# Kernel optimization log

Measured on AMD Instinct MI355X. Metric: run time of the kernel, lower is better.

The kernel has to match this reference:

```python
import jax, jax.numpy as jnp
import numpy as np

N, NFEAT, NHID, NCLASS, NLAYERS = 8192, 512, 128, 40, 3
NEG = -9e15

def _sparse_adj(key, n, density=0.002):
    u = jax.random.uniform(key, (n, n), dtype=jnp.float32)
    return jnp.where(u < density, u / density, 0.0)

def setup_inputs() -> dict:
    key = jax.random.key(0)
    ks = jax.random.split(key, 12)
    return {
        "x": jax.random.normal(ks[0], (N, NFEAT), dtype=jnp.float32),
        "adj1": _sparse_adj(ks[1], N),
        "adj2": _sparse_adj(ks[2], N),
        "adj_att": _sparse_adj(ks[3], N),
        "fc1_w": jax.random.normal(ks[4], (NLAYERS, NHID, NFEAT), dtype=jnp.float32) * (1.0 / np.sqrt(NFEAT)),
        "fc1_b": jnp.zeros((NLAYERS, NHID), jnp.float32),
        "Q_w": jax.random.normal(ks[5], (NLAYERS - 1, NHID, NHID), dtype=jnp.float32) * (1.0 / np.sqrt(NHID)),
        "Q_b": jnp.zeros((NLAYERS - 1, NHID), jnp.float32),
        "K_w": jax.random.normal(ks[6], (NLAYERS - 1, NHID, NHID), dtype=jnp.float32) * (1.0 / np.sqrt(NHID)),
        "K_b": jnp.zeros((NLAYERS - 1, NHID), jnp.float32),
        "hop_select": jnp.ones((NLAYERS,), jnp.float32),
        "w": jnp.ones((NLAYERS - 1, 2), jnp.float32),
        "clf_w": jax.random.normal(ks[7], (NCLASS, NHID * NLAYERS), dtype=jnp.float32) * (1.0 / np.sqrt(NHID * NLAYERS)),
        "clf_b": jnp.zeros((NCLASS,), jnp.float32),
    }

def _l2_normalize(x, eps=1e-12):
    # F.normalize(x, p=2, dim=1)
    n = jnp.sqrt(jnp.sum(x * x, axis=1, keepdims=True))
    return x / jnp.maximum(n, eps)

def reference(x, adj1, adj2, adj_att, fc1_w, fc1_b, Q_w, Q_b, K_w, K_b,
              hop_select, w, clf_w, clf_b):
    adj_list = [None, adj1, adj2]
    mask = jax.nn.softmax(hop_select)  # hop selection weights, shape [nlayers]
    outs = []
    for i in range(NLAYERS):
        tmp = x @ fc1_w[i].T + fc1_b[i]  # [N, nhid]
        if adj_list[i] is not None:
            adj = adj_list[i]
            W_att = jax.nn.softmax(w[i - 1])  # [2]
            tmp_att = adj_att @ tmp           # [N, nhid]
            # GCN1: linear then propagate with adj_att (act='None')
            Q = adj_att @ (tmp_att @ Q_w[i - 1].T + Q_b[i - 1])
            K = adj_att @ (tmp_att @ K_w[i - 1].T + K_b[i - 1])
            scores = Q @ K.T                  # [N, N]
            scores = jnp.where(adj > 0, scores, NEG)
            attention = jax.nn.softmax(scores, axis=-1) * W_att[0] + adj * W_att[1]
            tmp = attention @ tmp             # [N, nhid]
        tmp = _l2_normalize(tmp)
        outs.append(mask[i] * tmp)
    final = jnp.concatenate(outs, axis=1)     # [N, nhid*nlayers]
    out = jax.nn.relu(final) @ clf_w.T + clf_b  # dropout is identity in eval
    return jax.nn.log_softmax(out, axis=1)
```

## Files before the change

kernel.cpp:

```cpp
#include <hip/hip_runtime.h>
#include <hip/hip_bf16.h>

#define NN     8192
#define NF4    2048
#define NFEAT  512
#define NHID   128
#define NCLASS 40
#define NLAY   3
#define CAPA   128
#define FSZ    ((size_t)NN * NHID)

typedef float f32x4 __attribute__((ext_vector_type(4)));

__global__ __launch_bounds__(256, 4) void k_scan_fc1(
    const float* __restrict__ x, const float* __restrict__ fc1w, const float* __restrict__ fc1b,
    const float* __restrict__ adjA, const float* __restrict__ adj1, const float* __restrict__ adj2,
    const float* __restrict__ hop, const float* __restrict__ w,
    float* __restrict__ tmps, float* __restrict__ f_mask, float* __restrict__ f_watt,
    float* __restrict__ colsum, float* __restrict__ rowsumA,
    int* __restrict__ cnts, int* __restrict__ colsArr, float* __restrict__ valsArr)
{
    __shared__ float smem[6400];
    __shared__ int s_lcnt;
    __shared__ float s_lsum;
    const int bx = blockIdx.x, plane = blockIdx.y, tid = threadIdx.x;

    if (bx < 128) {
        float* As = smem;
        float* Bs = smem + 2176;
        const int tx = tid & 15, ty = tid >> 4;
        const int bm = bx * 64;
        const int layer = plane;
        const int bn = layer * 128;
        float acc[4][8] = {};

        for (int kt = 0; kt < NFEAT; kt += 32) {
            #pragma unroll
            for (int it = 0; it < 2; ++it) {
                int L = tid + it * 256;
                int r = L >> 3, c4 = (L & 7) * 4;
                f32x4 va = *reinterpret_cast<const f32x4*>(&x[(size_t)(bm + r) * NFEAT + kt + c4]);
                As[(c4 + 0) * 68 + r] = va[0];
                As[(c4 + 1) * 68 + r] = va[1];
                As[(c4 + 2) * 68 + r] = va[2];
                As[(c4 + 3) * 68 + r] = va[3];
            }
            #pragma unroll
            for (int it = 0; it < 4; ++it) {
                int L = tid + it * 256;
                int r = L >> 3, c4 = (L & 7) * 4;
                f32x4 vb = *reinterpret_cast<const f32x4*>(&fc1w[(size_t)(bn + r) * NFEAT + kt + c4]);
                Bs[(c4 + 0) * 132 + r] = vb[0];
                Bs[(c4 + 1) * 132 + r] = vb[1];
                Bs[(c4 + 2) * 132 + r] = vb[2];
                Bs[(c4 + 3) * 132 + r] = vb[3];
            }
            __syncthreads();
            #pragma unroll
            for (int kk = 0; kk < 32; ++kk) {
                f32x4 ra  = *reinterpret_cast<const f32x4*>(&As[kk * 68 + ty * 4]);
                f32x4 rb0 = *reinterpret_cast<const f32x4*>(&Bs[kk * 132 + tx * 4]);
                f32x4 rb1 = *reinterpret_cast<const f32x4*>(&Bs[kk * 132 + tx * 4 + 64]);
                #pragma unroll
                for (int i = 0; i < 4; ++i) {
                    #pragma unroll
                    for (int j = 0; j < 4; ++j) {
                        acc[i][j]     = fmaf(ra[i], rb0[j], acc[i][j]);
                        acc[i][j + 4] = fmaf(ra[i], rb1[j], acc[i][j + 4]);
                    }
                }
            }
            __syncthreads();
        }
        const float* bofs = fc1b + bn;
        #pragma unroll
        for (int i = 0; i < 4; ++i) {
            int m = bm + ty * 4 + i;
            #pragma unroll
            for (int j = 0; j < 8; ++j) {
                int lc = (j < 4) ? (tx * 4 + j) : (64 + tx * 4 + (j - 4));
                tmps[(size_t)layer * FSZ + (size_t)m * NHID + lc] = acc[i][j] + bofs[lc];
            }
        }
    } else if (bx < 128 + NN) {
        const int row = bx - 128, mat = plane;
        const float* adj = (mat == 0) ? adjA : (mat == 1 ? adj1 : adj2);
        if (tid == 0) { s_lcnt = 0; s_lsum = 0.f; }
        __syncthreads();
        const f32x4* arow = reinterpret_cast<const f32x4*>(adj + (size_t)row * NN);
        int* rc = colsArr + (size_t)(mat * NN + row) * CAPA;
        float* rv = valsArr + (size_t)(mat * NN + row) * CAPA;

        f32x4 v[8];
        #pragma unroll
        for (int i = 0; i < 8; ++i)
            v[i] = __builtin_nontemporal_load(&arow[tid + (i << 8)]);

        float ls = 0.f;
        #pragma unroll
        for (int i = 0; i < 8; ++i) {
            const int c4 = tid + (i << 8);
            #pragma unroll
            for (int k = 0; k < 4; ++k) {
                if (v[i][k] > 0.f) {
                    int p = atomicAdd(&s_lcnt, 1);
                    if (p < CAPA) { rc[p] = c4 * 4 + k; rv[p] = v[i][k]; }
                    ls += v[i][k];
                }
            }
        }
        if (mat == 0 && ls != 0.f) atomicAdd(&s_lsum, ls);
        __syncthreads();
        if (tid == 0) {
            cnts[mat * NN + row] = s_lcnt < CAPA ? s_lcnt : CAPA;
            if (mat == 0) rowsumA[row] = s_lsum;
        }
    } else if (plane == 0) {
        colsum[tid] = 0.f;
        if (tid == 0) {
            float m = fmaxf(fmaxf(hop[0], hop[1]), hop[2]);
            float e0 = expf(hop[0] - m), e1 = expf(hop[1] - m), e2 = expf(hop[2] - m);
            float s = e0 + e1 + e2;
            f_mask[0] = e0 / s; f_mask[1] = e1 / s; f_mask[2] = e2 / s;
            for (int l = 0; l < 2; ++l) {
                float a = w[2 * l], b = w[2 * l + 1];
                float mm = fmaxf(a, b);
                float ea = expf(a - mm), eb = expf(b - mm);
                float ss = ea + eb;
                f_watt[2 * l] = ea / ss; f_watt[2 * l + 1] = eb / ss;
            }
        }
    }
}

__global__ __launch_bounds__(128) void k_spmm_cs(
    const int* __restrict__ cnts, const int* __restrict__ colsArr, const float* __restrict__ valsArr,
    const float* __restrict__ tmps, float* __restrict__ tmp_att, float* __restrict__ colsum)
{
    int bx = blockIdx.x, L = blockIdx.y, t = threadIdx.x;
    if (bx >= NN) {
        int c = bx - NN;
        const float* X = tmps + (size_t)(L + 1) * FSZ + (size_t)c * 128 * NHID;
        float a = 0.f;
        for (int r = 0; r < 128; ++r) a += X[(size_t)r * NHID + t];
        atomicAdd(&colsum[L * NHID + t], a);
        return;
    }
    int row = bx;
    const float* X = tmps + (size_t)(L + 1) * FSZ;
    float* Y = tmp_att + (size_t)L * FSZ;
    __shared__ int sc[CAPA];
    __shared__ float sv[CAPA];
    int n = cnts[row];
    for (int p = t; p < n; p += 128) { sc[p] = colsArr[(size_t)row * CAPA + p]; sv[p] = valsArr[(size_t)row * CAPA + p]; }
    __syncthreads();
    float a0 = 0.f, a1 = 0.f, a2 = 0.f, a3 = 0.f;
    int p = 0;
    for (; p + 4 <= n; p += 4) {
        a0 = fmaf(sv[p],     X[(size_t)sc[p]     * NHID + t], a0);
        a1 = fmaf(sv[p + 1], X[(size_t)sc[p + 1] * NHID + t], a1);
        a2 = fmaf(sv[p + 2], X[(size_t)sc[p + 2] * NHID + t], a2);
        a3 = fmaf(sv[p + 3], X[(size_t)sc[p + 3] * NHID + t], a3);
    }
    for (; p < n; ++p) a0 = fmaf(sv[p], X[(size_t)sc[p] * NHID + t], a0);
    Y[(size_t)row * NHID + t] = (a0 + a1) + (a2 + a3);
}

__global__ __launch_bounds__(256, 2) void k_t2qkm(
    const int* __restrict__ cnts, const int* __restrict__ colsArr, const float* __restrict__ valsArr,
    const float* __restrict__ tmp_att, const float* __restrict__ Qw, const float* __restrict__ Kw,
    const float* __restrict__ Qb, const float* __restrict__ Kb,
    const float* __restrict__ rowsumA, float* __restrict__ QKm)
{
    __shared__ float AsT[128 * 64];
    __shared__ float Bs[128 * 64];
    const int tid = threadIdx.x;
    const int bm = blockIdx.x * 64, Lz = blockIdx.y;
    const float* X = tmp_att + (size_t)Lz * FSZ;

    {
        const int lrow = tid >> 2, coff = (tid & 3) * 32;
        const int row = bm + lrow;
        f32x4 acc[8] = {};
        const int n = cnts[row];
        const int* rc = colsArr + (size_t)row * CAPA;
        const float* rv = valsArr + (size_t)row * CAPA;
        for (int p = 0; p < n; ++p) {
            int c = rc[p];
            float v = rv[p];
            const f32x4* src = reinterpret_cast<const f32x4*>(X + (size_t)c * NHID + coff);
            #pragma unroll
            for (int j = 0; j < 8; ++j) {
                f32x4 s = src[j];
                acc[j][0] = fmaf(v, s[0], acc[j][0]);
                acc[j][1] = fmaf(v, s[1], acc[j][1]);
                acc[j][2] = fmaf(v, s[2], acc[j][2]);
                acc[j][3] = fmaf(v, s[3], acc[j][3]);
            }
        }
        #pragma unroll
        for (int j = 0; j < 8; ++j)
            #pragma unroll
            for (int q = 0; q < 4; ++q)
                AsT[(coff + j * 4 + q) * 64 + lrow] = acc[j][q];
    }
    __syncthreads();

    const int tx = tid & 15, ty = tid >> 4;
    float rs[4];
    #pragma unroll
    for (int i = 0; i < 4; ++i) rs[i] = rowsumA[bm + ty * 4 + i];
    float* C = QKm + (size_t)Lz * NN * 256;

    for (int ch = 0; ch < 4; ++ch) {
        const int bn = ch * 64;
        const float* Bp; const float* bp; int bc;
        if (bn < 128) { Bp = Qw + (size_t)Lz * NHID * NHID; bp = Qb + (size_t)Lz * NHID; bc = bn; }
        else          { Bp = Kw + (size_t)Lz * NHID * NHID; bp = Kb + (size_t)Lz * NHID; bc = bn - 128; }
        {
            int r = tid >> 2, c0 = (tid & 3) * 32;
            #pragma unroll
            for (int j = 0; j < 8; ++j) {
                f32x4 v = *reinterpret_cast<const f32x4*>(&Bp[(size_t)(bc + r) * NHID + c0 + j * 4]);
                #pragma unroll
                for (int q = 0; q < 4; ++q) Bs[(c0 + j * 4 + q) * 64 + r] = v[q];
            }
        }
        __syncthreads();
        float acc[4][4] = {};
        #pragma unroll 8
        for (int kk = 0; kk < 128; ++kk) {
            f32x4 ra = *reinterpret_cast<const f32x4*>(&AsT[kk * 64 + ty * 4]);
            f32x4 rb = *reinterpret_cast<const f32x4*>(&Bs[kk * 64 + tx * 4]);
            #pragma unroll
            for (int i = 0; i < 4; ++i)
                #pragma unroll
                for (int j = 0; j < 4; ++j)
                    acc[i][j] = fmaf(ra[i], rb[j], acc[i][j]);
        }
        #pragma unroll
        for (int i = 0; i < 4; ++i) {
            int m = bm + ty * 4 + i;
            #pragma unroll
            for (int j = 0; j < 4; ++j) {
                int nc = bn + tx * 4 + j;
                C[(size_t)m * 256 + nc] = acc[i][j] + rs[i] * bp[bc + tx * 4 + j];
            }
        }
        __syncthreads();
    }
}

__global__ __launch_bounds__(256) void k_attn(
    const int* __restrict__ cnts, const int* __restrict__ colsArr, const float* __restrict__ valsArr,
    const float* __restrict__ QKm, const float* __restrict__ tmps,
    const float* __restrict__ colsum, const float* __restrict__ watt,
    const float* __restrict__ mask, float* __restrict__ outsb)
{
    int row = blockIdx.x, L = blockIdx.y, t = threadIdx.x;
    const float* QK = QKm + (size_t)L * NN * 256;
    const float* T = tmps + (size_t)(L + 1) * FSZ;
    const int* rc = colsArr + (size_t)((1 + L) * NN + row) * CAPA;
    const float* rv = valsArr + (size_t)((1 + L) * NN + row) * CAPA;
    __shared__ int cols[CAPA];
    __shared__ float avals[CAPA];
    __shared__ float svals[CAPA];
    __shared__ __align__(16) float qrow[NHID];
    __shared__ float psum[2][NHID];
    __shared__ float ws[4];

    int n = cnts[(1 + L) * NN + row];
    for (int p = t; p < n; p += 256) { cols[p] = rc[p]; avals[p] = rv[p]; }
    if (t < 32) *reinterpret_cast<f32x4*>(&qrow[t * 4]) =
        *reinterpret_cast<const f32x4*>(QK + (size_t)row * 256 + t * 4);
    __syncthreads();

    float W0 = watt[L * 2], W1 = watt[L * 2 + 1];
    float acc = 0.f;

    if (n > 0) {
        int g = t >> 5, sl = t & 31;
        f32x4 qv = *reinterpret_cast<const f32x4*>(&qrow[sl * 4]);
        for (int p = g; p < n; p += 8) {
            f32x4 kv = *reinterpret_cast<const f32x4*>(QK + (size_t)cols[p] * 256 + 128 + sl * 4);
            float s = qv[0] * kv[0] + qv[1] * kv[1] + qv[2] * kv[2] + qv[3] * kv[3];
            #pragma unroll
            for (int m = 16; m; m >>= 1) s += __shfl_xor(s, m);
            if (sl == 0) svals[p] = s;
        }
        __syncthreads();
        if (t < 64) {
            float mx = -3.0e38f;
            for (int p = t; p < n; p += 64) mx = fmaxf(mx, svals[p]);
            #pragma unroll
            for (int m = 32; m; m >>= 1) mx = fmaxf(mx, __shfl_xor(mx, m));
            float ss = 0.f;
            for (int p = t; p < n; p += 64) ss += expf(svals[p] - mx);
            #pragma unroll
            for (int m = 32; m; m >>= 1) ss += __shfl_xor(ss, m);
            float inv = 1.0f / ss;
            for (int p = t; p < n; p += 64) avals[p] = expf(svals[p] - mx) * inv * W0 + avals[p] * W1;
        }
        __syncthreads();
        int half = t >> 7, tt = t & 127;
        float pacc = 0.f;
        for (int p = half; p < n; p += 2) pacc = fmaf(avals[p], T[(size_t)cols[p] * NHID + tt], pacc);
        psum[half][tt] = pacc;
        __syncthreads();
        if (t < 128) acc = psum[0][t] + psum[1][t];
    } else {
        if (t < 128) acc = W0 * (1.0f / (float)NN) * colsum[L * NHID + t];
    }

    float s2 = acc * acc;
    #pragma unroll
    for (int m = 32; m; m >>= 1) s2 += __shfl_xor(s2, m);
    if ((t & 63) == 0) ws[t >> 6] = s2;
    __syncthreads();
    if (t < 128) {
        float d = fmaxf(sqrtf(ws[0] + ws[1]), 1e-12f);
        outsb[(size_t)row * (NHID * NLAY) + (size_t)(L + 1) * NHID + t] = mask[L + 1] * acc / d;
    }
}

__global__ __launch_bounds__(128) void k_clf(
    const float* __restrict__ tmps0, const float* __restrict__ outs,
    const float* __restrict__ Wc, const float* __restrict__ bc,
    const float* __restrict__ mask, float* __restrict__ out)
{
    __shared__ float fin[2][NHID * NLAY];
    const int t = threadIdx.x, wv = t >> 6, lane = t & 63;
    const int row = blockIdx.x * 2 + wv;

    float v0 = tmps0[(size_t)row * NHID + lane];
    float v1 = tmps0[(size_t)row * NHID + 64 + lane];
    float s = v0 * v0 + v1 * v1;
    #pragma unroll
    for (int m = 32; m; m >>= 1) s += __shfl_xor(s, m);
    float d = fmaxf(sqrtf(s), 1e-12f);
    float m0 = mask[0];
    fin[wv][lane]      = fmaxf(m0 * v0 / d, 0.f);
    fin[wv][64 + lane] = fmaxf(m0 * v1 / d, 0.f);
    #pragma unroll
    for (int k = 0; k < 4; ++k)
        fin[wv][128 + k * 64 + lane] = fmaxf(outs[(size_t)row * (NHID * NLAY) + 128 + k * 64 + lane], 0.f);
    __syncthreads();

    float logit = -3.0e38f;
    if (lane < NCLASS) {
        const float* wrow = Wc + (size_t)lane * (NHID * NLAY);
        float a0 = 0.f, a1 = 0.f, a2 = 0.f, a3 = 0.f;
        #pragma unroll 4
        for (int k = 0; k < NHID * NLAY; k += 4) {
            a0 = fmaf(fin[wv][k],     wrow[k],     a0);
            a1 = fmaf(fin[wv][k + 1], wrow[k + 1], a1);
            a2 = fmaf(fin[wv][k + 2], wrow[k + 2], a2);
            a3 = fmaf(fin[wv][k + 3], wrow[k + 3], a3);
        }
        logit = bc[lane] + (a0 + a1) + (a2 + a3);
    }
    float mx = logit;
    #pragma unroll
    for (int m = 32; m; m >>= 1) mx = fmaxf(mx, __shfl_xor(mx, m));
    float e = (lane < NCLASS) ? expf(logit - mx) : 0.f;
    float ssum = e;
    #pragma unroll
    for (int m = 32; m; m >>= 1) ssum += __shfl_xor(ssum, m);
    if (lane < NCLASS) out[(size_t)row * NCLASS + lane] = logit - mx - logf(ssum);
}

extern "C" void kernel_launch(void* const* d_in, const int* in_sizes, int n_in,
                              void* d_out, int out_size, void* d_ws, size_t ws_size,
                              hipStream_t stream) {
    const float* x       = (const float*)d_in[0];
    const float* adj1    = (const float*)d_in[1];
    const float* adj2    = (const float*)d_in[2];
    const float* adj_att = (const float*)d_in[3];
    const float* fc1_w   = (const float*)d_in[4];
    const float* fc1_b   = (const float*)d_in[5];
    const float* Q_w     = (const float*)d_in[6];
    const float* Q_b     = (const float*)d_in[7];
    const float* K_w     = (const float*)d_in[8];
    const float* K_b     = (const float*)d_in[9];
    const float* hop     = (const float*)d_in[10];
    const float* w       = (const float*)d_in[11];
    const float* clf_w   = (const float*)d_in[12];
    const float* clf_b   = (const float*)d_in[13];

    float* W = (float*)d_ws;
    float* f_mask   = W;
    float* f_watt   = W + 4;
    float* f_colsum = W + 8;
    float* rowsumA  = W + 264;
    float* tmps     = W + 264 + NN;
    float* outsb    = tmps + 3 * FSZ;
    float* tmp_att  = outsb + 3 * FSZ;
    float* QKm      = tmp_att + 2 * FSZ;
    float* csr_vals = QKm + 4 * FSZ;
    int*   csr_cols = (int*)(csr_vals + 3 * FSZ);
    int*   csr_cnt  = csr_cols + 3 * FSZ;

    size_t need = (size_t)((char*)(csr_cnt + 3 * NN) - (char*)d_ws);
    if (ws_size < need) return;

    k_scan_fc1<<<dim3(NN + 129, 3), 256, 0, stream>>>(
        x, fc1_w, fc1_b, adj_att, adj1, adj2, hop, w,
        tmps, f_mask, f_watt, f_colsum, rowsumA, csr_cnt, csr_cols, csr_vals);

    k_spmm_cs<<<dim3(NN + 64, 2), 128, 0, stream>>>(
        csr_cnt, csr_cols, csr_vals, tmps, tmp_att, f_colsum);

    k_t2qkm<<<dim3(NN / 64, 2), 256, 0, stream>>>(
        csr_cnt, csr_cols, csr_vals, tmp_att, Q_w, K_w, Q_b, K_b, rowsumA, QKm);

    k_attn<<<dim3(NN, 2), 256, 0, stream>>>(
        csr_cnt, csr_cols, csr_vals, QKm, tmps, f_colsum, f_watt, f_mask, outsb);

    k_clf<<<NN / 2, 128, 0, stream>>>(tmps, outsb, clf_w, clf_b, f_mask, (float*)d_out);
}
```

Before: 356.4 us.

## Move adj1/adj2 scans into the QK stage and fuse attention with classifier

The first kernel now scans only adj_att alongside the fc1 GEMM, which uses a smaller K tile so it needs less shared memory. The adj1/adj2 compaction scans move into the QK-projection kernel, where they share one launch with that GEMM and overlap with it. The attention kernel handles both layers in one block per row and directly computes the classifier and log-softmax, which removes the outsb round trip and one launch. The cost is a more complex block-role dispatch, and the QK GEMM now reads weights straight from global memory instead of staging them in shared memory.

```diff
diff --git a/kernel.cpp b/kernel.cpp
--- a/kernel.cpp
+++ b/kernel.cpp
@@ -12,43 +12,36 @@
 
 typedef float f32x4 __attribute__((ext_vector_type(4)));
 
-__global__ __launch_bounds__(256, 4) void k_scan_fc1(
+__global__ __launch_bounds__(256, 4) void k_scanA_fc1(
     const float* __restrict__ x, const float* __restrict__ fc1w, const float* __restrict__ fc1b,
-    const float* __restrict__ adjA, const float* __restrict__ adj1, const float* __restrict__ adj2,
-    const float* __restrict__ hop, const float* __restrict__ w,
+    const float* __restrict__ adjA, const float* __restrict__ hop, const float* __restrict__ w,
     float* __restrict__ tmps, float* __restrict__ f_mask, float* __restrict__ f_watt,
     float* __restrict__ colsum, float* __restrict__ rowsumA,
     int* __restrict__ cnts, int* __restrict__ colsArr, float* __restrict__ valsArr)
 {
-    __shared__ float smem[6400];
-    __shared__ int s_lcnt;
-    __shared__ float s_lsum;
-    const int bx = blockIdx.x, plane = blockIdx.y, tid = threadIdx.x;
-
-    if (bx < 128) {
+    __shared__ float smem[3200];
+    const int bx = blockIdx.x, tid = threadIdx.x;
+
+    if (bx < 384) {
         float* As = smem;
-        float* Bs = smem + 2176;
+        float* Bs = smem + 1088;
         const int tx = tid & 15, ty = tid >> 4;
-        const int bm = bx * 64;
-        const int layer = plane;
+        const int bm = (bx & 127) * 64;
+        const int layer = bx >> 7;
         const int bn = layer * 128;
         float acc[4][8] = {};
 
-        for (int kt = 0; kt < NFEAT; kt += 32) {
+        const int rA = tid >> 2, cA = (tid & 3) * 4;
+        for (int kt = 0; kt < NFEAT; kt += 16) {
+            f32x4 va = *reinterpret_cast<const f32x4*>(&x[(size_t)(bm + rA) * NFEAT + kt + cA]);
+            As[(cA + 0) * 68 + rA] = va[0];
+            As[(cA + 1) * 68 + rA] = va[1];
+            As[(cA + 2) * 68 + rA] = va[2];
+            As[(cA + 3) * 68 + rA] = va[3];
             #pragma unroll
             for (int it = 0; it < 2; ++it) {
                 int L = tid + it * 256;
-                int r = L >> 3, c4 = (L & 7) * 4;
-                f32x4 va = *reinterpret_cast<const f32x4*>(&x[(size_t)(bm + r) * NFEAT + kt + c4]);
-                As[(c4 + 0) * 68 + r] = va[0];
-                As[(c4 + 1) * 68 + r] = va[1];
-                As[(c4 + 2) * 68 + r] = va[2];
-                As[(c4 + 3) * 68 + r] = va[3];
-            }
-            #pragma unroll
-            for (int it = 0; it < 4; ++it) {
-                int L = tid + it * 256;
-                int r = L >> 3, c4 = (L & 7) * 4;
+                int r = L >> 2, c4 = (L & 3) * 4;
                 f32x4 vb = *reinterpret_cast<const f32x4*>(&fc1w[(size_t)(bn + r) * NFEAT + kt + c4]);
                 Bs[(c4 + 0) * 132 + r] = vb[0];
                 Bs[(c4 + 1) * 132 + r] = vb[1];
@@ -57,7 +50,7 @@
             }
             __syncthreads();
             #pragma unroll
-            for (int kk = 0; kk < 32; ++kk) {
+            for (int kk = 0; kk < 16; ++kk) {
                 f32x4 ra  = *reinterpret_cast<const f32x4*>(&As[kk * 68 + ty * 4]);
                 f32x4 rb0 = *reinterpret_cast<const f32x4*>(&Bs[kk * 132 + tx * 4]);
                 f32x4 rb1 = *reinterpret_cast<const f32x4*>(&Bs[kk * 132 + tx * 4 + 64]);
@@ -82,19 +75,19 @@
                 tmps[(size_t)layer * FSZ + (size_t)m * NHID + lc] = acc[i][j] + bofs[lc];
             }
         }
-    } else if (bx < 128 + NN) {
-        const int row = bx - 128, mat = plane;
-        const float* adj = (mat == 0) ? adjA : (mat == 1 ? adj1 : adj2);
-        if (tid == 0) { s_lcnt = 0; s_lsum = 0.f; }
+    } else if (bx < 384 + NN) {
+        const int row = bx - 384;
+        int* s_lcnt = (int*)smem;
+        float* s_lsum = smem + 1;
+        if (tid == 0) { *s_lcnt = 0; *s_lsum = 0.f; }
         __syncthreads();
-        const f32x4* arow = reinterpret_cast<const f32x4*>(adj + (size_t)row * NN);
-        int* rc = colsArr + (size_t)(mat * NN + row) * CAPA;
-        float* rv = valsArr + (size_t)(mat * NN + row) * CAPA;
+        const f32x4* arow = reinterpret_cast<const f32x4*>(adjA + (size_t)row * NN);
+        int* rc = colsArr + (size_t)row * CAPA;
+        float* rv = valsArr + (size_t)row * CAPA;
 
         f32x4 v[8];
         #pragma unroll
-        for (int i = 0; i < 8; ++i)
-            v[i] = __builtin_nontemporal_load(&arow[tid + (i << 8)]);
+        for (int i = 0; i < 8; ++i) v[i] = arow[tid + (i << 8)];
 
         float ls = 0.f;
         #pragma unroll
@@ -103,19 +96,20 @@
             #pragma unroll
             for (int k = 0; k < 4; ++k) {
                 if (v[i][k] > 0.f) {
-                    int p = atomicAdd(&s_lcnt, 1);
+                    int p = atomicAdd(s_lcnt, 1);
                     if (p < CAPA) { rc[p] = c4 * 4 + k; rv[p] = v[i][k]; }
                     ls += v[i][k];
                 }
             }
         }
-        if (mat == 0 && ls != 0.f) atomicAdd(&s_lsum, ls);
+        if (ls != 0.f) atomicAdd(s_lsum, ls);
         __syncthreads();
         if (tid == 0) {
-            cnts[mat * NN + row] = s_lcnt < CAPA ? s_lcnt : CAPA;
-            if (mat == 0) rowsumA[row] = s_lsum;
-        }
-    } else if (plane == 0) {
+            int n = *s_lcnt;
+            cnts[row] = n < CAPA ? n : CAPA;
+            rowsumA[row] = *s_lsum;
+        }
+    } else {
         colsum[tid] = 0.f;
         if (tid == 0) {
             float m = fmaxf(fmaxf(hop[0], hop[1]), hop[2]);
@@ -166,207 +160,244 @@
     Y[(size_t)row * NHID + t] = (a0 + a1) + (a2 + a3);
 }
 
-__global__ __launch_bounds__(256, 2) void k_t2qkm(
+__global__ __launch_bounds__(256, 4) void k_scan12_t2(
     const int* __restrict__ cnts, const int* __restrict__ colsArr, const float* __restrict__ valsArr,
     const float* __restrict__ tmp_att, const float* __restrict__ Qw, const float* __restrict__ Kw,
     const float* __restrict__ Qb, const float* __restrict__ Kb,
-    const float* __restrict__ rowsumA, float* __restrict__ QKm)
+    const float* __restrict__ rowsumA, float* __restrict__ QKm,
+    const float* __restrict__ adj1, const float* __restrict__ adj2,
+    int* __restrict__ cntsOut, int* __restrict__ colsOut, float* __restrict__ valsOut)
 {
-    __shared__ float AsT[128 * 64];
-    __shared__ float Bs[128 * 64];
-    const int tid = threadIdx.x;
-    const int bm = blockIdx.x * 64, Lz = blockIdx.y;
-    const float* X = tmp_att + (size_t)Lz * FSZ;
-
-    {
-        const int lrow = tid >> 2, coff = (tid & 3) * 32;
-        const int row = bm + lrow;
-        f32x4 acc[8] = {};
-        const int n = cnts[row];
-        const int* rc = colsArr + (size_t)row * CAPA;
-        const float* rv = valsArr + (size_t)row * CAPA;
-        for (int p = 0; p < n; ++p) {
-            int c = rc[p];
-            float v = rv[p];
-            const f32x4* src = reinterpret_cast<const f32x4*>(X + (size_t)c * NHID + coff);
-            #pragma unroll
-            for (int j = 0; j < 8; ++j) {
-                f32x4 s = src[j];
-                acc[j][0] = fmaf(v, s[0], acc[j][0]);
-                acc[j][1] = fmaf(v, s[1], acc[j][1]);
-                acc[j][2] = fmaf(v, s[2], acc[j][2]);
-                acc[j][3] = fmaf(v, s[3], acc[j][3]);
-            }
-        }
-        #pragma unroll
-        for (int j = 0; j < 8; ++j)
-            #pragma unroll
-            for (int q = 0; q < 4; ++q)
-                AsT[(coff + j * 4 + q) * 64 + lrow] = acc[j][q];
-    }
-    __syncthreads();
-
-    const int tx = tid & 15, ty = tid >> 4;
-    float rs[4];
-    #pragma unroll
-    for (int i = 0; i < 4; ++i) rs[i] = rowsumA[bm + ty * 4 + i];
-    float* C = QKm + (size_t)Lz * NN * 256;
-
-    for (int ch = 0; ch < 4; ++ch) {
-        const int bn = ch * 64;
-        const float* Bp; const float* bp; int bc;
-        if (bn < 128) { Bp = Qw + (size_t)Lz * NHID * NHID; bp = Qb + (size_t)Lz * NHID; bc = bn; }
-        else          { Bp = Kw + (size_t)Lz * NHID * NHID; bp = Kb + (size_t)Lz * NHID; bc = bn - 128; }
+    __shared__ float AsT[8192];
+    const int b = blockIdx.x, tid = threadIdx.x;
+
+    if (b < 256) {
+        const int bm = (b & 127) * 64, Lz = b >> 7;
+        const float* X = tmp_att + (size_t)Lz * FSZ;
         {
-            int r = tid >> 2, c0 = (tid & 3) * 32;
-            #pragma unroll
-            for (int j = 0; j < 8; ++j) {
-                f32x4 v = *reinterpret_cast<const f32x4*>(&Bp[(size_t)(bc + r) * NHID + c0 + j * 4]);
-                #pragma unroll
-                for (int q = 0; q < 4; ++q) Bs[(c0 + j * 4 + q) * 64 + r] = v[q];
-            }
+            const int lrow = tid >> 2, coff = (tid & 3) * 32;
+            const int row = bm + lrow;
+            f32x4 acc[8] = {};
+            const int n = cnts[row];
+            const int* rc = colsArr + (size_t)row * CAPA;
+            const float* rv = valsArr + (size_t)row * CAPA;
+            for (int p = 0; p < n; ++p) {
+                int c = rc[p];
+                float v = rv[p];
+                const f32x4* src = reinterpret_cast<const f32x4*>(X + (size_t)c * NHID + coff);
+                #pragma unroll
+                for (int j = 0; j < 8; ++j) {
+                    f32x4 s = src[j];
+                    acc[j][0] = fmaf(v, s[0], acc[j][0]);
+                    acc[j][1] = fmaf(v, s[1], acc[j][1]);
+                    acc[j][2] = fmaf(v, s[2], acc[j][2]);
+                    acc[j][3] = fmaf(v, s[3], acc[j][3]);
+                }
+            }
+            #pragma unroll
+            for (int j = 0; j < 8; ++j)
+                #pragma unroll
+                for (int q = 0; q < 4; ++q)
+                    AsT[(coff + j * 4 + q) * 64 + lrow] = acc[j][q];
         }
         __syncthreads();
-        float acc[4][4] = {};
-        #pragma unroll 8
-        for (int kk = 0; kk < 128; ++kk) {
-            f32x4 ra = *reinterpret_cast<const f32x4*>(&AsT[kk * 64 + ty * 4]);
-            f32x4 rb = *reinterpret_cast<const f32x4*>(&Bs[kk * 64 + tx * 4]);
-            #pragma unroll
-            for (int i = 0; i < 4; ++i)
+
+        const int tx = tid & 15, ty = tid >> 4;
+        float rs[4];
+        #pragma unroll
+        for (int i = 0; i < 4; ++i) rs[i] = rowsumA[bm + ty * 4 + i];
+        float* C = QKm + (size_t)Lz * NN * 256;
+
+        #pragma unroll
+        for (int ch = 0; ch < 4; ++ch) {
+            const int bn = ch * 64;
+            const float* Bp; const float* bp; int bc;
+            if (bn < 128) { Bp = Qw + (size_t)Lz * NHID * NHID; bp = Qb + (size_t)Lz * NHID; bc = bn; }
+            else          { Bp = Kw + (size_t)Lz * NHID * NHID; bp = Kb + (size_t)Lz * NHID; bc = bn - 128; }
+            float acc[4][4] = {};
+            for (int k4 = 0; k4 < NHID; k4 += 4) {
+                f32x4 wv[4];
                 #pragma unroll
                 for (int j = 0; j < 4; ++j)
-                    acc[i][j] = fmaf(ra[i], rb[j], acc[i][j]);
-        }
-        #pragma unroll
-        for (int i = 0; i < 4; ++i) {
-            int m = bm + ty * 4 + i;
-            #pragma unroll
-            for (int j = 0; j < 4; ++j) {
-                int nc = bn + tx * 4 + j;
-                C[(size_t)m * 256 + nc] = acc[i][j] + rs[i] * bp[bc + tx * 4 + j];
-            }
-        }
+                    wv[j] = *reinterpret_cast<const f32x4*>(&Bp[(size_t)(bc + tx * 4 + j) * NHID + k4]);
+                #pragma unroll
+                for (int q = 0; q < 4; ++q) {
+                    f32x4 ra = *reinterpret_cast<const f32x4*>(&AsT[(k4 + q) * 64 + ty * 4]);
+                    #pragma unroll
+                    for (int i = 0; i < 4; ++i)
+                        #pragma unroll
+                        for (int j = 0; j < 4; ++j)
+                            acc[i][j] = fmaf(ra[i], wv[j][q], acc[i][j]);
+                }
+            }
+            #pragma unroll
+            for (int i = 0; i < 4; ++i) {
+                int m = bm + ty * 4 + i;
+                #pragma unroll
+                for (int j = 0; j < 4; ++j) {
+                    int nc = bn + tx * 4 + j;
+                    C[(size_t)m * 256 + nc] = acc[i][j] + rs[i] * bp[bc + tx * 4 + j];
+                }
+            }
+        }
+    } else {
+        const int e = b - 256;
+        const int mat = e >> 13, row = e & (NN - 1);
+        const float* adj = mat ? adj2 : adj1;
+        int* s_lcnt = (int*)AsT;
+        if (tid == 0) *s_lcnt = 0;
         __syncthreads();
+        const f32x4* arow = reinterpret_cast<const f32x4*>(adj + (size_t)row * NN);
+        int* rc = colsOut + (size_t)(mat * NN + row) * CAPA;
+        float* rv = valsOut + (size_t)(mat * NN + row) * CAPA;
+
+        f32x4 v[8];
+        #pragma unroll
+        for (int i = 0; i < 8; ++i) v[i] = arow[tid + (i << 8)];
+
+        #pragma unroll
+        for (int i = 0; i < 8; ++i) {
+            const int c4 = tid + (i << 8);
+            #pragma unroll
+            for (int k = 0; k < 4; ++k) {
+                if (v[i][k] > 0.f) {
+                    int p = atomicAdd(s_lcnt, 1);
+                    if (p < CAPA) { rc[p] = c4 * 4 + k; rv[p] = v[i][k]; }
+                }
+            }
+        }
+        __syncthreads();
+        if (tid == 0) {
+            int n = *s_lcnt;
+            cntsOut[mat * NN + row] = n < CAPA ? n : CAPA;
+        }
     }
 }
 
-__global__ __launch_bounds__(256) void k_attn(
-    const int* __restrict__ cnts, const int* __restrict__ colsArr, const float* __restrict__ valsArr,
+__global__ __launch_bounds__(256) void k_attn_clf(
+    const int* __restrict__ cnts12, const int* __restrict__ cols12, const float* __restrict__ vals12,
     const float* __restrict__ QKm, const float* __restrict__ tmps,
     const float* __restrict__ colsum, const float* __restrict__ watt,
-    const float* __restrict__ mask, float* __restrict__ outsb)
+    const float* __restrict__ mask, const float* __restrict__ Wc, const float* __restrict__ bc,
+    float* __restrict__ out)
 {
-    int row = blockIdx.x, L = blockIdx.y, t = threadIdx.x;
-    const float* QK = QKm + (size_t)L * NN * 256;
-    const float* T = tmps + (size_t)(L + 1) * FSZ;
-    const int* rc = colsArr + (size_t)((1 + L) * NN + row) * CAPA;
-    const float* rv = valsArr + (size_t)((1 + L) * NN + row) * CAPA;
-    __shared__ int cols[CAPA];
-    __shared__ float avals[CAPA];
-    __shared__ float svals[CAPA];
-    __shared__ __align__(16) float qrow[NHID];
-    __shared__ float psum[2][NHID];
+    const int row = blockIdx.x, t = threadIdx.x;
+    const int h = t >> 7, ht = t & 127;
+    __shared__ int cols[2][CAPA];
+    __shared__ float avals[2][CAPA];
+    __shared__ float svals[2][CAPA];
+    __shared__ __align__(16) float qrow[2][NHID];
     __shared__ float ws[4];
-
-    int n = cnts[(1 + L) * NN + row];
-    for (int p = t; p < n; p += 256) { cols[p] = rc[p]; avals[p] = rv[p]; }
-    if (t < 32) *reinterpret_cast<f32x4*>(&qrow[t * 4]) =
-        *reinterpret_cast<const f32x4*>(QK + (size_t)row * 256 + t * 4);
-    __syncthreads();
-
-    float W0 = watt[L * 2], W1 = watt[L * 2 + 1];
+    __shared__ float ws0[2];
+    __shared__ float fin[NHID * NLAY];
+    __shared__ float cpart[2][64];
+
+    const float* QK = QKm + (size_t)h * NN * 256;
+    const float* T = tmps + (size_t)(h + 1) * FSZ;
+    const int n = cnts12[h * NN + row];
+    const int* rc = cols12 + (size_t)(h * NN + row) * CAPA;
+    const float* rv = vals12 + (size_t)(h * NN + row) * CAPA;
+
+    for (int p = ht; p < n; p += 128) { cols[h][p] = rc[p]; avals[h][p] = rv[p]; }
+    if (ht < 32) *reinterpret_cast<f32x4*>(&qrow[h][ht * 4]) =
+        *reinterpret_cast<const f32x4*>(QK + (size_t)row * 256 + ht * 4);
+    __syncthreads();
+
+    const float W0 = watt[h * 2], W1 = watt[h * 2 + 1];
+
+    if (n > 0) {
+        int g = ht >> 5, sl = ht & 31;
+        f32x4 qv = *reinterpret_cast<const f32x4*>(&qrow[h][sl * 4]);
+        for (int p = g; p < n; p += 4) {
+            f32x4 kv = *reinterpret_cast<const f32x4*>(QK + (size_t)cols[h][p] * 256 + 128 + sl * 4);
+            float s = qv[0] * kv[0] + qv[1] * kv[1] + qv[2] * kv[2] + qv[3] * kv[3];
+            #pragma unroll
+            for (int m = 16; m; m >>= 1) s += __shfl_xor(s, m);
+            if (sl == 0) svals[h][p] = s;
+        }
+    }
+    __syncthreads();
+
+    if (n > 0 && ht < 64) {
+        float mx = -3.0e38f;
+        for (int p = ht; p < n; p += 64) mx = fmaxf(mx, svals[h][p]);
+        #pragma unroll
+        for (int m = 32; m; m >>= 1) mx = fmaxf(mx, __shfl_xor(mx, m));
+        float ss = 0.f;
+        for (int p = ht; p < n; p += 64) ss += expf(svals[h][p] - mx);
+        #pragma unroll
+        for (int m = 32; m; m >>= 1) ss += __shfl_xor(ss, m);
+        float inv = 1.0f / ss;
+        for (int p = ht; p < n; p += 64) avals[h][p] = expf(svals[h][p] - mx) * inv * W0 + avals[h][p] * W1;
+    }
+    __syncthreads();
+
     float acc = 0.f;
-
     if (n > 0) {
-        int g = t >> 5, sl = t & 31;
-        f32x4 qv = *reinterpret_cast<const f32x4*>(&qrow[sl * 4]);
-        for (int p = g; p < n; p += 8) {
-            f32x4 kv = *reinterpret_cast<const f32x4*>(QK + (size_t)cols[p] * 256 + 128 + sl * 4);
-            float s = qv[0] * kv[0] + qv[1] * kv[1] + qv[2] * kv[2] + qv[3] * kv[3];
-            #pragma unroll
-            for (int m = 16; m; m >>= 1) s += __shfl_xor(s, m);
-            if (sl == 0) svals[p] = s;
-        }
-        __syncthreads();
-        if (t < 64) {
-            float mx = -3.0e38f;
-            for (int p = t; p < n; p += 64) mx = fmaxf(mx, svals[p]);
-            #pragma unroll
-            for (int m = 32; m; m >>= 1) mx = fmaxf(mx, __shfl_xor(mx, m));
-            float ss = 0.f;
-            for (int p = t; p < n; p += 64) ss += expf(svals[p] - mx);
-            #pragma unroll
-            for (int m = 32; m; m >>= 1) ss += __shfl_xor(ss, m);
-            float inv = 1.0f / ss;
-            for (int p = t; p < n; p += 64) avals[p] = expf(svals[p] - mx) * inv * W0 + avals[p] * W1;
-        }
-        __syncthreads();
-        int half = t >> 7, tt = t & 127;
-        float pacc = 0.f;
-        for (int p = half; p < n; p += 2) pacc = fmaf(avals[p], T[(size_t)cols[p] * NHID + tt], pacc);
-        psum[half][tt] = pacc;
-        __syncthreads();
-        if (t < 128) acc = psum[0][t] + psum[1][t];
+        float a1 = 0.f;
+        int p = 0;
+        for (; p + 2 <= n; p += 2) {
+            acc = fmaf(avals[h][p],     T[(size_t)cols[h][p]     * NHID + ht], acc);
+            a1  = fmaf(avals[h][p + 1], T[(size_t)cols[h][p + 1] * NHID + ht], a1);
+        }
+        if (p < n) acc = fmaf(avals[h][p], T[(size_t)cols[h][p] * NHID + ht], acc);
+        acc += a1;
     } else {
-        if (t < 128) acc = W0 * (1.0f / (float)NN) * colsum[L * NHID + t];
+        acc = W0 * (1.0f / (float)NN) * colsum[h * NHID + ht];
     }
 
     float s2 = acc * acc;
     #pragma unroll
     for (int m = 32; m; m >>= 1) s2 += __shfl_xor(s2, m);
     if ((t & 63) == 0) ws[t >> 6] = s2;
-    __syncthreads();
+
+    float v0 = 0.f;
     if (t < 128) {
-        float d = fmaxf(sqrtf(ws[0] + ws[1]), 1e-12f);
-        outsb[(size_t)row * (NHID * NLAY) + (size_t)(L + 1) * NHID + t] = mask[L + 1] * acc / d;
-    }
-}
-
-__global__ __launch_bounds__(128) void k_clf(
-    const float* __restrict__ tmps0, const float* __restrict__ outs,
-    const float* __restrict__ Wc, const float* __restrict__ bc,
-    const float* __restrict__ mask, float* __restrict__ out)
-{
-    __shared__ float fin[2][NHID * NLAY];
-    const int t = threadIdx.x, wv = t >> 6, lane = t & 63;
-    const int row = blockIdx.x * 2 + wv;
-
-    float v0 = tmps0[(size_t)row * NHID + lane];
-    float v1 = tmps0[(size_t)row * NHID + 64 + lane];
-    float s = v0 * v0 + v1 * v1;
-    #pragma unroll
-    for (int m = 32; m; m >>= 1) s += __shfl_xor(s, m);
-    float d = fmaxf(sqrtf(s), 1e-12f);
-    float m0 = mask[0];
-    fin[wv][lane]      = fmaxf(m0 * v0 / d, 0.f);
-    fin[wv][64 + lane] = fmaxf(m0 * v1 / d, 0.f);
-    #pragma unroll
-    for (int k = 0; k < 4; ++k)
-        fin[wv][128 + k * 64 + lane] = fmaxf(outs[(size_t)row * (NHID * NLAY) + 128 + k * 64 + lane], 0.f);
-    __syncthreads();
-
-    float logit = -3.0e38f;
-    if (lane < NCLASS) {
-        const float* wrow = Wc + (size_t)lane * (NHID * NLAY);
+        v0 = tmps[(size_t)row * NHID + t];
+        float s0 = v0 * v0;
+        #pragma unroll
+        for (int m = 32; m; m >>= 1) s0 += __shfl_xor(s0, m);
+        if ((t & 63) == 0) ws0[t >> 6] = s0;
+    }
+    __syncthreads();
+
+    {
+        float d = fmaxf(sqrtf(ws[h * 2] + ws[h * 2 + 1]), 1e-12f);
+        fin[(h + 1) * NHID + ht] = fmaxf(mask[h + 1] * acc / d, 0.f);
+        if (t < 128) {
+            float d0 = fmaxf(sqrtf(ws0[0] + ws0[1]), 1e-12f);
+            fin[t] = fmaxf(mask[0] * v0 / d0, 0.f);
+        }
+    }
+    __syncthreads();
+
+    const int wv = t >> 6, lane = t & 63;
+    if (wv < 2 && lane < NCLASS) {
+        const float* wrow = Wc + (size_t)lane * (NHID * NLAY) + wv * 192;
+        const float* fi = fin + wv * 192;
         float a0 = 0.f, a1 = 0.f, a2 = 0.f, a3 = 0.f;
         #pragma unroll 4
-        for (int k = 0; k < NHID * NLAY; k += 4) {
-            a0 = fmaf(fin[wv][k],     wrow[k],     a0);
-            a1 = fmaf(fin[wv][k + 1], wrow[k + 1], a1);
-            a2 = fmaf(fin[wv][k + 2], wrow[k + 2], a2);
-            a3 = fmaf(fin[wv][k + 3], wrow[k + 3], a3);
-        }
-        logit = bc[lane] + (a0 + a1) + (a2 + a3);
-    }
-    float mx = logit;
-    #pragma unroll
-    for (int m = 32; m; m >>= 1) mx = fmaxf(mx, __shfl_xor(mx, m));
-    float e = (lane < NCLASS) ? expf(logit - mx) : 0.f;
-    float ssum = e;
-    #pragma unroll
-    for (int m = 32; m; m >>= 1) ssum += __shfl_xor(ssum, m);
-    if (lane < NCLASS) out[(size_t)row * NCLASS + lane] = logit - mx - logf(ssum);
+        for (int k = 0; k < 192; k += 4) {
+            a0 = fmaf(fi[k],     wrow[k],     a0);
+            a1 = fmaf(fi[k + 1], wrow[k + 1], a1);
+            a2 = fmaf(fi[k + 2], wrow[k + 2], a2);
+            a3 = fmaf(fi[k + 3], wrow[k + 3], a3);
+        }
+        cpart[wv][lane] = (a0 + a1) + (a2 + a3);
+    }
+    __syncthreads();
+
+    if (t < 64) {
+        float logit = (t < NCLASS) ? (cpart[0][t] + cpart[1][t] + bc[t]) : -3.0e38f;
+        float mx = logit;
+        #pragma unroll
+        for (int m = 32; m; m >>= 1) mx = fmaxf(mx, __shfl_xor(mx, m));
+        float e = (t < NCLASS) ? expf(logit - mx) : 0.f;
+        float ssum = e;
+        #pragma unroll
+        for (int m = 32; m; m >>= 1) ssum += __shfl_xor(ssum, m);
+        if (t < NCLASS) out[(size_t)row * NCLASS + t] = logit - mx - logf(ssum);
+    }
 }
 
 extern "C" void kernel_launch(void* const* d_in, const int* in_sizes, int n_in,
@@ -393,28 +424,30 @@
     float* f_colsum = W + 8;
     float* rowsumA  = W + 264;
     float* tmps     = W + 264 + NN;
-    float* outsb    = tmps + 3 * FSZ;
-    float* tmp_att  = outsb + 3 * FSZ;
+    float* tmp_att  = tmps + 3 * FSZ;
     float* QKm      = tmp_att + 2 * FSZ;
-    float* csr_vals = QKm + 4 * FSZ;
-    int*   csr_cols = (int*)(csr_vals + 3 * FSZ);
-    int*   csr_cnt  = csr_cols + 3 * FSZ;
-
-    size_t need = (size_t)((char*)(csr_cnt + 3 * NN) - (char*)d_ws);
+    float* csr_valsA = QKm + 4 * FSZ;
+    float* csr_vals12 = csr_valsA + FSZ;
+    int*   csr_colsA = (int*)(csr_vals12 + 2 * FSZ);
+    int*   csr_cols12 = csr_colsA + FSZ;
+    int*   csr_cntA  = csr_cols12 + 2 * FSZ;
+    int*   csr_cnt12 = csr_cntA + NN;
+
+    size_t need = (size_t)((char*)(csr_cnt12 + 2 * NN) - (char*)d_ws);
     if (ws_size < need) return;
 
-    k_scan_fc1<<<dim3(NN + 129, 3), 256, 0, stream>>>(
-        x, fc1_w, fc1_b, adj_att, adj1, adj2, hop, w,
-        tmps, f_mask, f_watt, f_colsum, rowsumA, csr_cnt, csr_cols, csr_vals);
+    k_scanA_fc1<<<384 + NN + 1, 256, 0, stream>>>(
+        x, fc1_w, fc1_b, adj_att, hop, w,
+        tmps, f_mask, f_watt, f_colsum, rowsumA, csr_cntA, csr_colsA, csr_valsA);
 
     k_spmm_cs<<<dim3(NN + 64, 2), 128, 0, stream>>>(
-        csr_cnt, csr_cols, csr_vals, tmps, tmp_att, f_colsum);
-
-    k_t2qkm<<<dim3(NN / 64, 2), 256, 0, stream>>>(
-        csr_cnt, csr_cols, csr_vals, tmp_att, Q_w, K_w, Q_b, K_b, rowsumA, QKm);
-
-    k_attn<<<dim3(NN, 2), 256, 0, stream>>>(
-        csr_cnt, csr_cols, csr_vals, QKm, tmps, f_colsum, f_watt, f_mask, outsb);
-
-    k_clf<<<NN / 2, 128, 0, stream>>>(tmps, outsb, clf_w, clf_b, f_mask, (float*)d_out);
+        csr_cntA, csr_colsA, csr_valsA, tmps, tmp_att, f_colsum);
+
+    k_scan12_t2<<<256 + 2 * NN, 256, 0, stream>>>(
+        csr_cntA, csr_colsA, csr_valsA, tmp_att, Q_w, K_w, Q_b, K_b, rowsumA, QKm,
+        adj1, adj2, csr_cnt12, csr_cols12, csr_vals12);
+
+    k_attn_clf<<<NN, 256, 0, stream>>>(
+        csr_cnt12, csr_cols12, csr_vals12, QKm, tmps, f_colsum, f_watt, f_mask,
+        clf_w, clf_b, (float*)d_out);
 }
```

New measurement: 339.7 us. -4.7%, faster.
